# Optimization experiments

Measured on AMD Instinct MI355X. Metric: run time of the kernel, lower is better.

The kernel has to match this reference:

```python
import jax, jax.numpy as jnp
import numpy as np

N, F_IN, H, C, D, NH, L, FF = 4096, 256, 2, 64, 128, 4, 2, 2048
DEG = 32


def setup_inputs() -> dict:
    key = jax.random.key(0)
    ks = jax.random.split(key, 32)
    s = 0.05
    # graph: random edges + self loops (PyG GATConv adds self loops)
    src = jax.random.randint(ks[0], (N * DEG,), 0, N)
    dst = jax.random.randint(ks[1], (N * DEG,), 0, N)
    loop = jnp.arange(N)
    edge_index = jnp.stack([jnp.concatenate([src, loop]),
                            jnp.concatenate([dst, loop])]).astype(jnp.int64)
    inp = {
        'x': jax.random.normal(ks[2], (N, F_IN), jnp.float32),
        'edge_index': edge_index,
        'enc_w1': jax.random.normal(ks[3], (F_IN, 128), jnp.float32) * s,
        'enc_b1': jnp.zeros((128,), jnp.float32),
        'enc_w2': jax.random.normal(ks[4], (128, D), jnp.float32) * s,
        'enc_b2': jnp.zeros((D,), jnp.float32),
        'gat_w': jax.random.normal(ks[5], (D, H * C), jnp.float32) * s,
        'gat_asrc': jax.random.normal(ks[6], (H, C), jnp.float32) * s,
        'gat_adst': jax.random.normal(ks[7], (H, C), jnp.float32) * s,
        'gat_bias': jnp.zeros((H * C,), jnp.float32),
        't_wq': jax.random.normal(ks[8], (L, D, D), jnp.float32) * s,
        't_bq': jnp.zeros((L, D), jnp.float32),
        't_wk': jax.random.normal(ks[9], (L, D, D), jnp.float32) * s,
        't_bk': jnp.zeros((L, D), jnp.float32),
        't_wv': jax.random.normal(ks[10], (L, D, D), jnp.float32) * s,
        't_bv': jnp.zeros((L, D), jnp.float32),
        't_wo': jax.random.normal(ks[11], (L, D, D), jnp.float32) * s,
        't_bo': jnp.zeros((L, D), jnp.float32),
        't_ln1_g': jnp.ones((L, D), jnp.float32),
        't_ln1_b': jnp.zeros((L, D), jnp.float32),
        't_ln2_g': jnp.ones((L, D), jnp.float32),
        't_ln2_b': jnp.zeros((L, D), jnp.float32),
        't_w1': jax.random.normal(ks[12], (L, D, FF), jnp.float32) * s,
        't_b1': jnp.zeros((L, FF), jnp.float32),
        't_w2': jax.random.normal(ks[13], (L, FF, D), jnp.float32) * s,
        't_b2': jnp.zeros((L, D), jnp.float32),
    }
    return inp


def _layer_norm(v, g, b):
    m = v.mean(-1, keepdims=True)
    var = v.var(-1, keepdims=True)
    return (v - m) / jnp.sqrt(var + 1e-5) * g + b


def _forward(x, edge_index, enc_w1, enc_b1, enc_w2, enc_b2,
             gat_w, gat_asrc, gat_adst, gat_bias,
             t_wq, t_bq, t_wk, t_bk, t_wv, t_bv, t_wo, t_bo,
             t_ln1_g, t_ln1_b, t_ln2_g, t_ln2_b, t_w1, t_b1, t_w2, t_b2):
    n = x.shape[0]
    # encoder MLP: Linear -> ReLU -> Linear
    h = jnp.maximum(x @ enc_w1 + enc_b1, 0.0) @ enc_w2 + enc_b2  # [N, D]
    # GATConv (concat heads), dropout inactive (eval)
    heads, ch = gat_asrc.shape
    hh = (h @ gat_w).reshape(n, heads, ch)                       # [N, H, C]
    src, dst = edge_index[0], edge_index[1]
    a_src = (hh * gat_asrc).sum(-1)                              # [N, H]
    a_dst = (hh * gat_adst).sum(-1)
    e = jax.nn.leaky_relu(a_src[src] + a_dst[dst], 0.2)          # [E, H]
    # segment softmax over destination nodes
    e_max = jax.ops.segment_max(e, dst, num_segments=n)
    e_exp = jnp.exp(e - e_max[dst])
    denom = jax.ops.segment_sum(e_exp, dst, num_segments=n)
    alpha = e_exp / denom[dst]                                   # [E, H]
    agg = jax.ops.segment_sum(alpha[:, :, None] * hh[src], dst, num_segments=n)
    y = agg.reshape(n, heads * ch) + gat_bias                    # [N, D]
    # TransformerEncoder (post-LN, relu FFN), unbatched sequence of N nodes
    d = y.shape[-1]
    dh = d // NH
    for l in range(t_wq.shape[0]):
        q = (y @ t_wq[l] + t_bq[l]).reshape(n, NH, dh)
        k = (y @ t_wk[l] + t_bk[l]).reshape(n, NH, dh)
        v = (y @ t_wv[l] + t_bv[l]).reshape(n, NH, dh)
        scores = jnp.einsum('nhd,mhd->hnm', q, k) / jnp.sqrt(jnp.float32(dh))
        p = jax.nn.softmax(scores, axis=-1)
        a = jnp.einsum('hnm,mhd->nhd', p, v).reshape(n, d)
        a = a @ t_wo[l] + t_bo[l]
        y = _layer_norm(y + a, t_ln1_g[l], t_ln1_b[l])
        f = jnp.maximum(y @ t_w1[l] + t_b1[l], 0.0) @ t_w2[l] + t_b2[l]
        y = _layer_norm(y + f, t_ln2_g[l], t_ln2_b[l])
    return y


def reference(x, edge_index, enc_w1, enc_b1, enc_w2, enc_b2,
              gat_w, gat_asrc, gat_adst, gat_bias,
              t_wq, t_bq, t_wk, t_bk, t_wv, t_bv, t_wo, t_bo,
              t_ln1_g, t_ln1_b, t_ln2_g, t_ln2_b, t_w1, t_b1, t_w2, t_b2):
    return _forward(x, edge_index, enc_w1, enc_b1, enc_w2, enc_b2,
                    gat_w, gat_asrc, gat_adst, gat_bias,
                    t_wq, t_bq, t_wk, t_bk, t_wv, t_bv, t_wo, t_bo,
                    t_ln1_g, t_ln1_b, t_ln2_g, t_ln2_b, t_w1, t_b1, t_w2, t_b2)
```

## Files before the change

kernel.cpp:

```cpp
#include <hip/hip_runtime.h>

typedef unsigned short u16;
typedef unsigned int u32;
typedef __attribute__((ext_vector_type(8))) short bh8;
typedef __attribute__((ext_vector_type(4))) float fx4;
typedef __attribute__((ext_vector_type(4))) short s4;
typedef __attribute__((ext_vector_type(2))) unsigned int u32x2;

#define QS 0.2550437194342803f

__device__ __forceinline__ u16 f2bf(float f) {
    unsigned u = __float_as_uint(f);
    u += 0x7fffu + ((u >> 16) & 1u);
    return (u16)(u >> 16);
}

__device__ __forceinline__ u32 cvtpk(float lo, float hi) {
    u32 r;
    asm("v_cvt_pk_bf16_f32 %0, %1, %2" : "=v"(r) : "v"(lo), "v"(hi));
    return r;
}

__global__ __launch_bounds__(256) void prep_kernel(
    const float* x, const float* ew1, const float* ew2, const float* gw,
    const float* wq, const float* wk, const float* wv, const float* wo,
    const float* w1, const float* w2,
    const float* bq, const float* bk, const float* bv,
    u16* xb, u16* ew1t, u16* ew2t, u16* gwt,
    u16* wqkvt, float* bqkv, u16* wot, u16* w1t, u16* w2t)
{
    __shared__ u16 tile[64 * 65];
    int bid = blockIdx.x;
    const int t = threadIdx.x;

    if (bid < 128) {
        const float4* x4 = (const float4*)x;
        s4* o4 = (s4*)xb;
        #pragma unroll
        for (int i = 0; i < 8; i++) {
            int fi = bid * 2048 + i * 256 + t;
            float4 v = x4[fi];
            s4 o = { (short)f2bf(v.x), (short)f2bf(v.y), (short)f2bf(v.z), (short)f2bf(v.w) };
            o4[fi] = o;
        }
        return;
    }
    bid -= 128;
    if (bid < 1) {
        for (int idx = t; idx < 768; idx += 256) {
            int l = idx / 384, n = idx % 384;
            float v;
            if (n < 128)      v = bq[l * 128 + n] * QS;
            else if (n < 256) v = bk[l * 128 + n - 128];
            else              v = bv[l * 128 + n - 256];
            bqkv[idx] = v;
        }
        return;
    }
    bid -= 1;

    const float* src; u16* dst; int R, C, tr, tc; float sc = 1.f;
    if (bid < 8)            { src = ew1; dst = ew1t; R = 256; C = 128; tr = bid >> 1; tc = bid & 1; }
    else if ((bid -= 8) < 4)  { src = ew2; dst = ew2t; R = 128; C = 128; tr = bid >> 1; tc = bid & 1; }
    else if ((bid -= 4) < 4)  { src = gw;  dst = gwt;  R = 128; C = 128; tr = bid >> 1; tc = bid & 1; }
    else if ((bid -= 4) < 24) {
        int l = bid / 12, r2 = bid % 12, which = r2 >> 2, i = r2 & 3;
        R = 128; C = 128; tr = i >> 1; tc = i & 1;
        if (which == 0)      { src = wq + l * 16384; dst = wqkvt + l * 49152;         sc = QS; }
        else if (which == 1) { src = wk + l * 16384; dst = wqkvt + l * 49152 + 16384; }
        else                 { src = wv + l * 16384; dst = wqkvt + l * 49152 + 32768; }
    }
    else if ((bid -= 24) < 8)   { int l = bid >> 2, i = bid & 3;  src = wo + l * 16384; dst = wot + l * 16384; R = 128; C = 128; tr = i >> 1; tc = i & 1; }
    else if ((bid -= 8) < 128)  { int l = bid >> 6, i = bid & 63; src = w1 + (size_t)l * 262144; dst = w1t + (size_t)l * 262144; R = 128;  C = 2048; tr = i & 1;  tc = i >> 1; }
    else { bid -= 128;            int l = bid >> 6, i = bid & 63; src = w2 + (size_t)l * 262144; dst = w2t + (size_t)l * 262144; R = 2048; C = 128;  tr = i >> 1; tc = i & 1; }

    const int r = t >> 2, cs = (t & 3) * 16;
    const float* sp = src + (size_t)(tr * 64 + r) * C + tc * 64 + cs;
    #pragma unroll
    for (int j = 0; j < 16; j++) tile[r * 65 + cs + j] = f2bf(sp[j] * sc);
    __syncthreads();
    u16* dp = dst + (size_t)(tc * 64 + r) * R + tr * 64 + cs;
    #pragma unroll
    for (int j = 0; j < 16; j++) dp[j] = tile[(cs + j) * 65 + r];
}

__global__ __launch_bounds__(256) void gemm_bf16(
    const u16* __restrict__ A, const u16* __restrict__ Bt,
    const float* __restrict__ bias,
    float* __restrict__ Cf, u16* __restrict__ Cb, float* __restrict__ Cpart,
    u16* __restrict__ Cvt,
    int M, int N, int K, int relu, int kchunk, int ldc)
{
    __shared__ __align__(16) u16 As[2][64][40];
    __shared__ __align__(16) u16 Bs[2][64][40];
    const int m0 = blockIdx.x * 64, n0 = blockIdx.y * 64, z = blockIdx.z;
    const int tid = threadIdx.x;
    const int lane = tid & 63, w = tid >> 6;
    const int wm = (w >> 1) * 32, wn = (w & 1) * 32;
    const int l15 = lane & 15, l4 = lane >> 4;
    const int srow = tid >> 2, skq = (tid & 3) * 8;
    const int k0 = z * kchunk;

    const u16* Ap = A + (size_t)(m0 + srow) * K + k0 + skq;
    const u16* Bp = Bt + (size_t)(n0 + srow) * K + k0 + skq;

    fx4 acc00 = {0,0,0,0}, acc01 = {0,0,0,0}, acc10 = {0,0,0,0}, acc11 = {0,0,0,0};

    *(int4*)&As[0][srow][skq] = *(const int4*)Ap;
    *(int4*)&Bs[0][srow][skq] = *(const int4*)Bp;

    const int niter = kchunk >> 5;
    for (int it = 0; it < niter; it++) {
        const int cur = it & 1;
        int4 ar, br;
        __syncthreads();
        if (it + 1 < niter) {
            ar = *(const int4*)(Ap + (it + 1) * 32);
            br = *(const int4*)(Bp + (it + 1) * 32);
        }
        bh8 a0 = *(const bh8*)&As[cur][wm + l15][l4 * 8];
        bh8 a1 = *(const bh8*)&As[cur][wm + 16 + l15][l4 * 8];
        bh8 b0 = *(const bh8*)&Bs[cur][wn + l15][l4 * 8];
        bh8 b1 = *(const bh8*)&Bs[cur][wn + 16 + l15][l4 * 8];
        acc00 = __builtin_amdgcn_mfma_f32_16x16x32_bf16(a0, b0, acc00, 0, 0, 0);
        acc01 = __builtin_amdgcn_mfma_f32_16x16x32_bf16(a0, b1, acc01, 0, 0, 0);
        acc10 = __builtin_amdgcn_mfma_f32_16x16x32_bf16(a1, b0, acc10, 0, 0, 0);
        acc11 = __builtin_amdgcn_mfma_f32_16x16x32_bf16(a1, b1, acc11, 0, 0, 0);
        if (it + 1 < niter) {
            *(int4*)&As[cur ^ 1][srow][skq] = ar;
            *(int4*)&Bs[cur ^ 1][srow][skq] = br;
        }
    }

    fx4* accs[2][2] = {{&acc00, &acc01}, {&acc10, &acc11}};
    #pragma unroll
    for (int i = 0; i < 2; i++)
        #pragma unroll
        for (int j = 0; j < 2; j++) {
            int colg = n0 + wn + j * 16 + l15;
            int rowb = m0 + wm + i * 16 + l4 * 4;
            if (Cpart) {
                float* cp = Cpart + (size_t)z * M * N;
                #pragma unroll
                for (int r = 0; r < 4; r++)
                    cp[(size_t)(rowb + r) * N + colg] = (*accs[i][j])[r];
                continue;
            }
            float bvv = bias ? bias[colg] : 0.f;
            float vals[4];
            #pragma unroll
            for (int r = 0; r < 4; r++) {
                float v = (*accs[i][j])[r] + bvv;
                vals[r] = relu ? fmaxf(v, 0.f) : v;
            }
            if (Cvt && colg >= 256) {
                s4 pk = { (short)f2bf(vals[0]), (short)f2bf(vals[1]),
                          (short)f2bf(vals[2]), (short)f2bf(vals[3]) };
                *(s4*)&Cvt[(size_t)(colg - 256) * 4096 + rowb] = pk;
            } else {
                #pragma unroll
                for (int r = 0; r < 4; r++) {
                    if (Cf) Cf[(size_t)(rowb + r) * ldc + colg] = vals[r];
                    if (Cb) Cb[(size_t)(rowb + r) * ldc + colg] = f2bf(vals[r]);
                }
            }
        }
}

__global__ __launch_bounds__(128) void gat_prep(
    const float* __restrict__ hh, const float* __restrict__ asrc,
    const float* __restrict__ adst, float* __restrict__ an_src,
    float* __restrict__ an_dst, int* __restrict__ counts)
{
    int n = blockIdx.x, tid = threadIdx.x;
    if (tid == 0) counts[n] = 0;
    int head = tid >> 6, c = tid & 63;
    float v = hh[n * 128 + tid];
    float ps = v * asrc[head * 64 + c];
    float pd = v * adst[head * 64 + c];
    for (int off = 32; off; off >>= 1) { ps += __shfl_down(ps, off); pd += __shfl_down(pd, off); }
    if (c == 0) { an_src[n * 2 + head] = ps; an_dst[n * 2 + head] = pd; }
}

__global__ void count_edges(const int* __restrict__ dst, int* counts, int E) {
    int i = blockIdx.x * 256 + threadIdx.x;
    if (i < E) atomicAdd(&counts[dst[i]], 1);
}

__global__ __launch_bounds__(1024) void scan_kernel(const int* __restrict__ counts,
                                                    int* row_start, int* cursor) {
    __shared__ int wsum[16];
    int tid = threadIdx.x, lane = tid & 63, wv = tid >> 6;
    int b = tid * 4;
    int c0 = counts[b], c1 = counts[b+1], c2 = counts[b+2], c3 = counts[b+3];
    int sum = c0 + c1 + c2 + c3;
    int inc = sum;
    #pragma unroll
    for (int off = 1; off < 64; off <<= 1) {
        int v = __shfl_up(inc, off);
        if (lane >= off) inc += v;
    }
    if (lane == 63) wsum[wv] = inc;
    __syncthreads();
    int base = 0;
    #pragma unroll
    for (int i = 0; i < 16; i++) {
        int v = wsum[i];
        base += (i < wv) ? v : 0;
    }
    int excl = base + inc - sum;
    int r0 = excl, r1 = excl + c0, r2 = r1 + c1, r3 = r2 + c2;
    row_start[b] = r0; row_start[b+1] = r1; row_start[b+2] = r2; row_start[b+3] = r3;
    cursor[b] = r0; cursor[b+1] = r1; cursor[b+2] = r2; cursor[b+3] = r3;
    if (tid == 1023) row_start[4096] = base + inc;
}

__global__ void scatter_edges(const int* __restrict__ src, const int* __restrict__ dst,
                              int* cursor, int* csr_src, int E) {
    int i = blockIdx.x * 256 + threadIdx.x;
    if (i < E) { int pos = atomicAdd(&cursor[dst[i]], 1); csr_src[pos] = src[i]; }
}

__global__ __launch_bounds__(256) void gat_aggregate(
    const int* __restrict__ row_start, const int* __restrict__ csr_src,
    const float* __restrict__ an_src, const float* __restrict__ an_dst,
    const float* __restrict__ hh, const float* __restrict__ gbias,
    float* __restrict__ y32, u16* __restrict__ yb)
{
    int n = blockIdx.x, tid = threadIdx.x;
    const int lane = tid & 63, wv = tid >> 6;
    int start = row_start[n], end = row_start[n + 1];
    float ad0 = an_dst[n * 2 + 0], ad1 = an_dst[n * 2 + 1];
    __shared__ float rmx[4][2], rsm[4][2];
    __shared__ float sal0[128], sal1[128], sagg[256];
    __shared__ int sidx[128];

    float mx0 = -1e30f, mx1 = -1e30f;
    for (int i = start + tid; i < end; i += 256) {
        int s = csr_src[i];
        float e0 = an_src[s * 2 + 0] + ad0; e0 = e0 > 0.f ? e0 : 0.2f * e0;
        float e1 = an_src[s * 2 + 1] + ad1; e1 = e1 > 0.f ? e1 : 0.2f * e1;
        mx0 = fmaxf(mx0, e0); mx1 = fmaxf(mx1, e1);
    }
    for (int off = 32; off; off >>= 1) { mx0 = fmaxf(mx0, __shfl_down(mx0, off)); mx1 = fmaxf(mx1, __shfl_down(mx1, off)); }
    if (lane == 0) { rmx[wv][0] = mx0; rmx[wv][1] = mx1; }
    __syncthreads();
    mx0 = fmaxf(fmaxf(rmx[0][0], rmx[1][0]), fmaxf(rmx[2][0], rmx[3][0]));
    mx1 = fmaxf(fmaxf(rmx[0][1], rmx[1][1]), fmaxf(rmx[2][1], rmx[3][1]));

    float den0 = 0.f, den1 = 0.f;
    for (int i = start + tid; i < end; i += 256) {
        int s = csr_src[i];
        float e0 = an_src[s * 2 + 0] + ad0; e0 = e0 > 0.f ? e0 : 0.2f * e0;
        float e1 = an_src[s * 2 + 1] + ad1; e1 = e1 > 0.f ? e1 : 0.2f * e1;
        den0 += __expf(e0 - mx0); den1 += __expf(e1 - mx1);
    }
    for (int off = 32; off; off >>= 1) { den0 += __shfl_down(den0, off); den1 += __shfl_down(den1, off); }
    if (lane == 0) { rsm[wv][0] = den0; rsm[wv][1] = den1; }
    __syncthreads();
    den0 = rsm[0][0] + rsm[1][0] + rsm[2][0] + rsm[3][0];
    den1 = rsm[0][1] + rsm[1][1] + rsm[2][1] + rsm[3][1];
    float rd0 = 1.f / den0, rd1 = 1.f / den1;

    const int grp = tid >> 7, ch = tid & 127, head = ch >> 6;
    float agg = 0.f;
    for (int c0 = start; c0 < end; c0 += 128) {
        int cnt = min(128, end - c0);
        __syncthreads();
        if (tid < cnt) {
            int s = csr_src[c0 + tid];
            float e0 = an_src[s * 2 + 0] + ad0; e0 = e0 > 0.f ? e0 : 0.2f * e0;
            float e1 = an_src[s * 2 + 1] + ad1; e1 = e1 > 0.f ? e1 : 0.2f * e1;
            sal0[tid] = __expf(e0 - mx0) * rd0;
            sal1[tid] = __expf(e1 - mx1) * rd1;
            sidx[tid] = s;
        }
        __syncthreads();
        const float* sal = head ? sal1 : sal0;
        for (int j = grp; j < cnt; j += 2)
            agg += sal[j] * hh[(size_t)sidx[j] * 128 + ch];
    }
    sagg[tid] = agg;
    __syncthreads();
    if (tid < 128) {
        float v = sagg[tid] + sagg[tid + 128] + gbias[tid];
        y32[(size_t)n * 128 + tid] = v;
        yb[(size_t)n * 128 + tid] = f2bf(v);
    }
}

__global__ __launch_bounds__(256) void flash_attn_part(
    const u16* __restrict__ q, const u16* __restrict__ k,
    const u16* __restrict__ vt, float* __restrict__ po,
    float* __restrict__ pm, float* __restrict__ pl)
{
    __shared__ __align__(16) u16 Kb[2][64][40];
    __shared__ __align__(16) u16 Vb[2][32][72];
    __shared__ __align__(16) u16 Ps[4][16][72];
    const int q0 = blockIdx.x * 64, h = blockIdx.y, ch = blockIdx.z;
    const int tid = threadIdx.x;
    const int w = tid >> 6, lane = tid & 63, l15 = lane & 15, l4 = lane >> 4;

    bh8 qf = *(const bh8*)&q[(size_t)(q0 + w * 16 + l15) * 256 + h * 32 + l4 * 8];

    const int skey = tid >> 2, sds = (tid & 3) * 8;
    const int svd = tid >> 3, svk = (tid & 7) * 8;
    const u16* kgp = &k[(size_t)(ch * 512 + skey) * 256 + h * 32 + sds];
    const u16* vgp = &vt[(size_t)(h * 32 + svd) * 4096 + ch * 512 + svk];

    fx4 o0 = {0,0,0,0}, o1 = {0,0,0,0};
    float M = -1e30f, L = 0.f;

    *(int4*)&Kb[0][skey][sds] = *(const int4*)kgp;
    *(int4*)&Vb[0][svd][svk] = *(const int4*)vgp;

    for (int ti = 0; ti < 8; ti++) {
        const int cur = ti & 1;
        int4 kr, vr;
        __syncthreads();
        if (ti < 7) {
            kr = *(const int4*)(kgp + (size_t)(ti + 1) * 64 * 256);
            vr = *(const int4*)(vgp + (ti + 1) * 64);
        }

        fx4 s[4];
        #pragma unroll
        for (int sub = 0; sub < 4; sub++) {
            bh8 kf = *(const bh8*)&Kb[cur][sub * 16 + l15][l4 * 8];
            fx4 z = {0,0,0,0};
            s[sub] = __builtin_amdgcn_mfma_f32_16x16x32_bf16(kf, qf, z, 0, 0, 0);
        }
        float t0 = fmaxf(fmaxf(s[0][0], s[0][1]), s[0][2]);
        float t1 = fmaxf(fmaxf(s[0][3], s[1][0]), s[1][1]);
        float t2 = fmaxf(fmaxf(s[1][2], s[1][3]), s[2][0]);
        float t3 = fmaxf(fmaxf(s[2][1], s[2][2]), s[2][3]);
        float t4 = fmaxf(fmaxf(s[3][0], s[3][1]), s[3][2]);
        float pmax = fmaxf(fmaxf(fmaxf(t0, t1), t2), fmaxf(fmaxf(t3, t4), s[3][3]));
        pmax = fmaxf(pmax, __shfl_xor(pmax, 16));
        pmax = fmaxf(pmax, __shfl_xor(pmax, 32));
        if (!__all(pmax - M <= 8.0f)) {
            float f = __builtin_amdgcn_exp2f(M - pmax);
            M = pmax;
            o0 *= f; o1 *= f; L *= f;
        }

        #pragma unroll
        for (int sub = 0; sub < 4; sub++)
            #pragma unroll
            for (int r = 0; r < 4; r++)
                s[sub][r] = __builtin_amdgcn_exp2f(s[sub][r] - M);
        float ss0 = (s[0][0] + s[0][1]) + (s[0][2] + s[0][3]);
        float ss1 = (s[1][0] + s[1][1]) + (s[1][2] + s[1][3]);
        float ss2 = (s[2][0] + s[2][1]) + (s[2][2] + s[2][3]);
        float ss3 = (s[3][0] + s[3][1]) + (s[3][2] + s[3][3]);
        float lsum = (ss0 + ss1) + (ss2 + ss3);
        lsum += __shfl_xor(lsum, 16);
        lsum += __shfl_xor(lsum, 32);
        L += lsum;

        #pragma unroll
        for (int sub = 0; sub < 4; sub++) {
            u32x2 pk = { cvtpk(s[sub][0], s[sub][1]), cvtpk(s[sub][2], s[sub][3]) };
            *(u32x2*)&Ps[w][l15][sub * 16 + l4 * 4] = pk;
        }

        #pragma unroll
        for (int kc = 0; kc < 2; kc++) {
            bh8 bf  = *(const bh8*)&Ps[w][l15][kc * 32 + l4 * 8];
            bh8 af0 = *(const bh8*)&Vb[cur][l15][kc * 32 + l4 * 8];
            bh8 af1 = *(const bh8*)&Vb[cur][16 + l15][kc * 32 + l4 * 8];
            o0 = __builtin_amdgcn_mfma_f32_16x16x32_bf16(af0, bf, o0, 0, 0, 0);
            o1 = __builtin_amdgcn_mfma_f32_16x16x32_bf16(af1, bf, o1, 0, 0, 0);
        }

        if (ti < 7) {
            *(int4*)&Kb[cur ^ 1][skey][sds] = kr;
            *(int4*)&Vb[cur ^ 1][svd][svk] = vr;
        }
    }
    const int base = (blockIdx.x * 4 + h) * 8 + ch;
    const int qrow = w * 16 + l15;
    *(fx4*)&po[(size_t)(base * 64 + qrow) * 32 + l4 * 4]      = o0;
    *(fx4*)&po[(size_t)(base * 64 + qrow) * 32 + 16 + l4 * 4] = o1;
    if (l4 == 0) { pm[base * 64 + qrow] = M; pl[base * 64 + qrow] = L; }
}

__global__ __launch_bounds__(256) void attn_combine(
    const float* __restrict__ po, const float* __restrict__ pm,
    const float* __restrict__ pl, u16* __restrict__ out)
{
    int qb = blockIdx.x, h = blockIdx.y;
    int col = threadIdx.x & 31, r0 = threadIdx.x >> 5;
    int rb = (qb * 4 + h) * 8;
    for (int j = 0; j < 8; j++) {
        int row = r0 * 8 + j;
        float m = -1e30f;
        for (int c = 0; c < 8; c++) m = fmaxf(m, pm[(rb + c) * 64 + row]);
        float l = 0.f, o = 0.f;
        for (int c = 0; c < 8; c++) {
            float wgt = __builtin_amdgcn_exp2f(pm[(rb + c) * 64 + row] - m);
            l += wgt * pl[(rb + c) * 64 + row];
            o += wgt * po[(size_t)((rb + c) * 64 + row) * 32 + col];
        }
        out[(size_t)(qb * 64 + row) * 128 + h * 32 + col] = f2bf(o / l);
    }
}

__global__ __launch_bounds__(256) void oproj_ln(
    const u16* __restrict__ A, const u16* __restrict__ Bt,
    const float* __restrict__ bias, const float* __restrict__ g,
    const float* __restrict__ b,
    float* __restrict__ y32, u16* __restrict__ yb)
{
    __shared__ __align__(16) u16 As[2][32][40];
    __shared__ __align__(16) u16 Bs[2][128][40];
    __shared__ float Ct[32][132];
    const int m0 = blockIdx.x * 32;
    const int tid = threadIdx.x;
    const int lane = tid & 63, w = tid >> 6;
    const int wm = (w >> 1) * 16, wn = (w & 1) * 64;
    const int l15 = lane & 15, l4 = lane >> 4;

    const int arow = tid >> 2, akq = (tid & 3) * 8;
    const u16* Ap  = A + (size_t)(m0 + arow) * 128 + akq;
    const u16* Bp0 = Bt + (size_t)arow * 128 + akq;
    const u16* Bp1 = Bp0 + (size_t)64 * 128;

    fx4 acc[4] = {};

    if (tid < 128) *(int4*)&As[0][arow][akq] = *(const int4*)Ap;
    *(int4*)&Bs[0][arow][akq]      = *(const int4*)Bp0;
    *(int4*)&Bs[0][arow + 64][akq] = *(const int4*)Bp1;

    for (int it = 0; it < 4; it++) {
        const int cur = it & 1;
        int4 ar, br0, br1;
        __syncthreads();
        if (it < 3) {
            if (tid < 128) ar = *(const int4*)(Ap + (it + 1) * 32);
            br0 = *(const int4*)(Bp0 + (it + 1) * 32);
            br1 = *(const int4*)(Bp1 + (it + 1) * 32);
        }
        bh8 af = *(const bh8*)&As[cur][wm + l15][l4 * 8];
        #pragma unroll
        for (int nj = 0; nj < 4; nj++) {
            bh8 bf = *(const bh8*)&Bs[cur][wn + nj * 16 + l15][l4 * 8];
            acc[nj] = __builtin_amdgcn_mfma_f32_16x16x32_bf16(af, bf, acc[nj], 0, 0, 0);
        }
        if (it < 3) {
            if (tid < 128) *(int4*)&As[cur ^ 1][arow][akq] = ar;
            *(int4*)&Bs[cur ^ 1][arow][akq]      = br0;
            *(int4*)&Bs[cur ^ 1][arow + 64][akq] = br1;
        }
    }

    #pragma unroll
    for (int nj = 0; nj < 4; nj++) {
        int cl = wn + nj * 16 + l15;
        float bvv = bias[cl];
        #pragma unroll
        for (int r = 0; r < 4; r++) {
            int rl = wm + l4 * 4 + r;
            Ct[rl][cl] = acc[nj][r] + bvv + y32[(size_t)(m0 + rl) * 128 + cl];
        }
    }
    __syncthreads();

    const int row = tid >> 3, c0 = (tid & 7) * 16;
    float s1 = 0.f, s2 = 0.f;
    #pragma unroll
    for (int j = 0; j < 16; j++) { float v = Ct[row][c0 + j]; s1 += v; s2 += v * v; }
    #pragma unroll
    for (int off = 1; off < 8; off <<= 1) { s1 += __shfl_xor(s1, off); s2 += __shfl_xor(s2, off); }
    float mean = s1 * (1.f / 128.f);
    float var = s2 * (1.f / 128.f) - mean * mean;
    float rstd = rsqrtf(var + 1e-5f);
    #pragma unroll
    for (int j = 0; j < 16; j++) {
        int col = c0 + j;
        float o = (Ct[row][col] - mean) * rstd * g[col] + b[col];
        y32[(size_t)(m0 + row) * 128 + col] = o;
        yb[(size_t)(m0 + row) * 128 + col] = f2bf(o);
    }
}

__global__ __launch_bounds__(128) void add_ln_p(
    const float* __restrict__ y, const float* __restrict__ part, int nz,
    const float* __restrict__ bias,
    const float* __restrict__ g, const float* __restrict__ b,
    float* __restrict__ out32, u16* __restrict__ outb)
{
    int n = blockIdx.x, tid = threadIdx.x;
    float v = y[(size_t)n * 128 + tid] + bias[tid];
    for (int z = 0; z < nz; z++) v += part[(size_t)z * 524288 + n * 128 + tid];
    float sacc = v;
    for (int off = 32; off; off >>= 1) sacc += __shfl_down(sacc, off);
    __shared__ float sm[2], sv[2];
    if ((tid & 63) == 0) sm[tid >> 6] = sacc;
    __syncthreads();
    float mean = (sm[0] + sm[1]) * (1.f / 128.f);
    float d = v - mean;
    float qacc = d * d;
    for (int off = 32; off; off >>= 1) qacc += __shfl_down(qacc, off);
    if ((tid & 63) == 0) sv[tid >> 6] = qacc;
    __syncthreads();
    float var = (sv[0] + sv[1]) * (1.f / 128.f);
    float o = d * rsqrtf(var + 1e-5f) * g[tid] + b[tid];
    out32[(size_t)n * 128 + tid] = o;
    outb[(size_t)n * 128 + tid] = f2bf(o);
}

extern "C" void kernel_launch(void* const* d_in, const int* in_sizes, int n_in,
                              void* d_out, int out_size, void* d_ws, size_t ws_size,
                              hipStream_t stream)
{
    const float* x     = (const float*)d_in[0];
    const int*   ei    = (const int*)  d_in[1];
    const float* ew1   = (const float*)d_in[2];
    const float* eb1   = (const float*)d_in[3];
    const float* ew2   = (const float*)d_in[4];
    const float* eb2   = (const float*)d_in[5];
    const float* gw    = (const float*)d_in[6];
    const float* gasrc = (const float*)d_in[7];
    const float* gadst = (const float*)d_in[8];
    const float* gbias = (const float*)d_in[9];
    const float* wq    = (const float*)d_in[10];
    const float* bq    = (const float*)d_in[11];
    const float* wk    = (const float*)d_in[12];
    const float* bk    = (const float*)d_in[13];
    const float* wv    = (const float*)d_in[14];
    const float* bv    = (const float*)d_in[15];
    const float* wo    = (const float*)d_in[16];
    const float* bo    = (const float*)d_in[17];
    const float* ln1g  = (const float*)d_in[18];
    const float* ln1b  = (const float*)d_in[19];
    const float* ln2g  = (const float*)d_in[20];
    const float* ln2b  = (const float*)d_in[21];
    const float* w1    = (const float*)d_in[22];
    const float* b1    = (const float*)d_in[23];
    const float* w2    = (const float*)d_in[24];
    const float* b2    = (const float*)d_in[25];

    const int E = in_sizes[1] / 2;
    const int* esrc = ei;
    const int* edst = ei + E;

    char* p = (char*)d_ws;
    auto alloc = [&](size_t bytes) -> void* {
        void* r = (void*)p;
        p += (bytes + 255) & ~(size_t)255;
        return r;
    };
    u16* xb    = (u16*)alloc(4096 * 256 * 2);
    u16* ew1t  = (u16*)alloc(128 * 256 * 2);
    u16* ew2t  = (u16*)alloc(128 * 128 * 2);
    u16* gwt   = (u16*)alloc(128 * 128 * 2);
    u16* wqkvt = (u16*)alloc(2 * 384 * 128 * 2);
    float* bqkv = (float*)alloc(2 * 384 * 4);
    u16* wot   = (u16*)alloc(2 * 128 * 128 * 2);
    u16* w1t   = (u16*)alloc(2 * 2048 * 128 * 2);
    u16* w2t   = (u16*)alloc(2 * 128 * 2048 * 2);
    u16* h1b   = (u16*)alloc(4096 * 128 * 2);
    u16* hb    = (u16*)alloc(4096 * 128 * 2);
    float* hh  = (float*)alloc(4096 * 128 * 4);
    float* ansrc = (float*)alloc(4096 * 2 * 4);
    float* andst = (float*)alloc(4096 * 2 * 4);
    int* counts    = (int*)alloc(4096 * 4);
    int* row_start = (int*)alloc(4097 * 4);
    int* cursor    = (int*)alloc(4096 * 4);
    int* csr_src   = (int*)alloc((size_t)E * 4);
    float* y32 = (float*)alloc(4096 * 128 * 4);
    u16* yb    = (u16*)alloc(4096 * 128 * 2);
    u16* qkvb  = (u16*)alloc((size_t)4096 * 256 * 2);
    u16* vtb   = (u16*)alloc(4096 * 128 * 2);
    u16* attnb = (u16*)alloc(4096 * 128 * 2);
    float* po  = (float*)alloc((size_t)64 * 4 * 8 * 64 * 32 * 4);
    float* pm  = (float*)alloc(64 * 4 * 8 * 64 * 4);
    float* pl  = (float*)alloc(64 * 4 * 8 * 64 * 4);
    u16* ff1b  = (u16*)alloc((size_t)4096 * 2048 * 2);
    float* ff2part = (float*)alloc((size_t)4 * 4096 * 128 * 4);

    prep_kernel<<<433, 256, 0, stream>>>(x, ew1, ew2, gw, wq, wk, wv, wo, w1, w2,
                                         bq, bk, bv,
                                         xb, ew1t, ew2t, gwt, wqkvt, bqkv, wot, w1t, w2t);

    gemm_bf16<<<dim3(64, 2), 256, 0, stream>>>(xb, ew1t, eb1, nullptr, h1b, nullptr, nullptr, 4096, 128, 256, 1, 256, 128);
    gemm_bf16<<<dim3(64, 2), 256, 0, stream>>>(h1b, ew2t, eb2, nullptr, hb, nullptr, nullptr, 4096, 128, 128, 0, 128, 128);

    gemm_bf16<<<dim3(64, 2), 256, 0, stream>>>(hb, gwt, nullptr, hh, nullptr, nullptr, nullptr, 4096, 128, 128, 0, 128, 128);
    gat_prep<<<4096, 128, 0, stream>>>(hh, gasrc, gadst, ansrc, andst, counts);
    count_edges<<<(E + 255) / 256, 256, 0, stream>>>(edst, counts, E);
    scan_kernel<<<1, 1024, 0, stream>>>(counts, row_start, cursor);
    scatter_edges<<<(E + 255) / 256, 256, 0, stream>>>(esrc, edst, cursor, csr_src, E);
    gat_aggregate<<<4096, 256, 0, stream>>>(row_start, csr_src, ansrc, andst, hh, gbias, y32, yb);

    for (int l = 0; l < 2; l++) {
        gemm_bf16<<<dim3(64, 6), 256, 0, stream>>>(yb, wqkvt + l * 49152, bqkv + l * 384, nullptr, qkvb, nullptr, vtb, 4096, 384, 128, 0, 128, 256);
        flash_attn_part<<<dim3(64, 4, 8), 256, 0, stream>>>(qkvb, qkvb + 128, vtb, po, pm, pl);
        attn_combine<<<dim3(64, 4), 256, 0, stream>>>(po, pm, pl, attnb);
        oproj_ln<<<128, 256, 0, stream>>>(attnb, wot + l * 16384, bo + l * 128, ln1g + l * 128, ln1b + l * 128, y32, yb);
        gemm_bf16<<<dim3(64, 32), 256, 0, stream>>>(yb, w1t + (size_t)l * 262144, b1 + l * 2048, nullptr, ff1b, nullptr, nullptr, 4096, 2048, 128, 1, 128, 2048);
        gemm_bf16<<<dim3(64, 2, 4), 256, 0, stream>>>(ff1b, w2t + (size_t)l * 262144, nullptr, nullptr, nullptr, ff2part, nullptr, 4096, 128, 2048, 0, 512, 128);
        float* outp = (l == 1) ? (float*)d_out : y32;
        add_ln_p<<<4096, 128, 0, stream>>>(y32, ff2part, 4, b2 + l * 128, ln2g + l * 128, ln2b + l * 128, outp, yb);
    }
}
```

Before: 199.6 us.

## Fuse FFN up/down projections into one kernel and halve attention key splits

Adds an ffn_fused kernel in which each block keeps a 64-row activation tile in LDS. It computes ReLU(yW1+b1) for 64-wide FF chunks into shared memory and multiplies them directly by W2, writing 8 split-K partial sums. This removes the 4096x2048 bf16 intermediate round-trip to global memory and one launch, but W2 fragments are read straight from global and the partial-sum traffic doubles. Separately, flash attention now uses 4 key chunks of 1024 instead of 8 of 512, which cuts combine work and partial buffers but halves grid parallelism.

```diff
diff --git a/kernel.cpp b/kernel.cpp
--- a/kernel.cpp
+++ b/kernel.cpp
@@ -167,6 +167,94 @@
         }
 }
 
+__global__ __launch_bounds__(256) void ffn_fused(
+    const u16* __restrict__ A, const u16* __restrict__ W1t,
+    const float* __restrict__ b1, const u16* __restrict__ W2t,
+    float* __restrict__ part)
+{
+    __shared__ __align__(16) u16 Ab[64][136];
+    __shared__ __align__(16) u16 Wb[64][136];
+    __shared__ __align__(16) u16 Sb[64][72];
+    const int m0 = blockIdx.x * 64, z = blockIdx.y;
+    const int tid = threadIdx.x;
+    const int lane = tid & 63, w = tid >> 6;
+    const int wm = (w >> 1) * 32;
+    const int wn = (w & 1) * 32;
+    const int wn2 = (w & 1) * 64;
+    const int l15 = lane & 15, l4 = lane >> 4;
+    const int sr = tid >> 2, sc = (tid & 3) * 32;
+
+    {
+        const u16* ap = A + (size_t)(m0 + sr) * 128 + sc;
+        #pragma unroll
+        for (int i = 0; i < 4; i++)
+            *(int4*)&Ab[sr][sc + i * 8] = *(const int4*)(ap + i * 8);
+    }
+
+    fx4 acc2[2][4] = {};
+
+    for (int chunk = 0; chunk < 4; chunk++) {
+        const int ffbase = z * 256 + chunk * 64;
+        __syncthreads();
+        {
+            const u16* wp = W1t + (size_t)(ffbase + sr) * 128 + sc;
+            #pragma unroll
+            for (int i = 0; i < 4; i++)
+                *(int4*)&Wb[sr][sc + i * 8] = *(const int4*)(wp + i * 8);
+        }
+        __syncthreads();
+
+        fx4 s[2][2] = {};
+        #pragma unroll
+        for (int ks = 0; ks < 4; ks++) {
+            bh8 af0 = *(const bh8*)&Ab[wm + l15][ks * 32 + l4 * 8];
+            bh8 af1 = *(const bh8*)&Ab[wm + 16 + l15][ks * 32 + l4 * 8];
+            bh8 bf0 = *(const bh8*)&Wb[wn + l15][ks * 32 + l4 * 8];
+            bh8 bf1 = *(const bh8*)&Wb[wn + 16 + l15][ks * 32 + l4 * 8];
+            s[0][0] = __builtin_amdgcn_mfma_f32_16x16x32_bf16(af0, bf0, s[0][0], 0, 0, 0);
+            s[0][1] = __builtin_amdgcn_mfma_f32_16x16x32_bf16(af0, bf1, s[0][1], 0, 0, 0);
+            s[1][0] = __builtin_amdgcn_mfma_f32_16x16x32_bf16(af1, bf0, s[1][0], 0, 0, 0);
+            s[1][1] = __builtin_amdgcn_mfma_f32_16x16x32_bf16(af1, bf1, s[1][1], 0, 0, 0);
+        }
+        #pragma unroll
+        for (int mi = 0; mi < 2; mi++)
+            #pragma unroll
+            for (int nj = 0; nj < 2; nj++) {
+                float bv = b1[ffbase + wn + nj * 16 + l15];
+                #pragma unroll
+                for (int r = 0; r < 4; r++) {
+                    float v = fmaxf(s[mi][nj][r] + bv, 0.f);
+                    Sb[wm + mi * 16 + l4 * 4 + r][wn + nj * 16 + l15] = f2bf(v);
+                }
+            }
+        __syncthreads();
+
+        #pragma unroll
+        for (int ks = 0; ks < 2; ks++) {
+            bh8 af0 = *(const bh8*)&Sb[wm + l15][ks * 32 + l4 * 8];
+            bh8 af1 = *(const bh8*)&Sb[wm + 16 + l15][ks * 32 + l4 * 8];
+            #pragma unroll
+            for (int nj = 0; nj < 4; nj++) {
+                bh8 bf = *(const bh8*)&W2t[(size_t)(wn2 + nj * 16 + l15) * 2048 + ffbase + ks * 32 + l4 * 8];
+                acc2[0][nj] = __builtin_amdgcn_mfma_f32_16x16x32_bf16(af0, bf, acc2[0][nj], 0, 0, 0);
+                acc2[1][nj] = __builtin_amdgcn_mfma_f32_16x16x32_bf16(af1, bf, acc2[1][nj], 0, 0, 0);
+            }
+        }
+    }
+
+    float* cp = part + (size_t)z * 524288;
+    #pragma unroll
+    for (int mi = 0; mi < 2; mi++)
+        #pragma unroll
+        for (int nj = 0; nj < 4; nj++) {
+            int colg = wn2 + nj * 16 + l15;
+            int rowb = m0 + wm + mi * 16 + l4 * 4;
+            #pragma unroll
+            for (int r = 0; r < 4; r++)
+                cp[(size_t)(rowb + r) * 128 + colg] = acc2[mi][nj][r];
+        }
+}
+
 __global__ __launch_bounds__(128) void gat_prep(
     const float* __restrict__ hh, const float* __restrict__ asrc,
     const float* __restrict__ adst, float* __restrict__ an_src,
@@ -305,8 +393,8 @@
 
     const int skey = tid >> 2, sds = (tid & 3) * 8;
     const int svd = tid >> 3, svk = (tid & 7) * 8;
-    const u16* kgp = &k[(size_t)(ch * 512 + skey) * 256 + h * 32 + sds];
-    const u16* vgp = &vt[(size_t)(h * 32 + svd) * 4096 + ch * 512 + svk];
+    const u16* kgp = &k[(size_t)(ch * 1024 + skey) * 256 + h * 32 + sds];
+    const u16* vgp = &vt[(size_t)(h * 32 + svd) * 4096 + ch * 1024 + svk];
 
     fx4 o0 = {0,0,0,0}, o1 = {0,0,0,0};
     float M = -1e30f, L = 0.f;
@@ -314,11 +402,11 @@
     *(int4*)&Kb[0][skey][sds] = *(const int4*)kgp;
     *(int4*)&Vb[0][svd][svk] = *(const int4*)vgp;
 
-    for (int ti = 0; ti < 8; ti++) {
+    for (int ti = 0; ti < 16; ti++) {
         const int cur = ti & 1;
         int4 kr, vr;
         __syncthreads();
-        if (ti < 7) {
+        if (ti < 15) {
             kr = *(const int4*)(kgp + (size_t)(ti + 1) * 64 * 256);
             vr = *(const int4*)(vgp + (ti + 1) * 64);
         }
@@ -373,12 +461,12 @@
             o1 = __builtin_amdgcn_mfma_f32_16x16x32_bf16(af1, bf, o1, 0, 0, 0);
         }
 
-        if (ti < 7) {
+        if (ti < 15) {
             *(int4*)&Kb[cur ^ 1][skey][sds] = kr;
             *(int4*)&Vb[cur ^ 1][svd][svk] = vr;
         }
     }
-    const int base = (blockIdx.x * 4 + h) * 8 + ch;
+    const int base = (blockIdx.x * 4 + h) * 4 + ch;
     const int qrow = w * 16 + l15;
     *(fx4*)&po[(size_t)(base * 64 + qrow) * 32 + l4 * 4]      = o0;
     *(fx4*)&po[(size_t)(base * 64 + qrow) * 32 + 16 + l4 * 4] = o1;
@@ -391,13 +479,13 @@
 {
     int qb = blockIdx.x, h = blockIdx.y;
     int col = threadIdx.x & 31, r0 = threadIdx.x >> 5;
-    int rb = (qb * 4 + h) * 8;
+    int rb = (qb * 4 + h) * 4;
     for (int j = 0; j < 8; j++) {
         int row = r0 * 8 + j;
         float m = -1e30f;
-        for (int c = 0; c < 8; c++) m = fmaxf(m, pm[(rb + c) * 64 + row]);
+        for (int c = 0; c < 4; c++) m = fmaxf(m, pm[(rb + c) * 64 + row]);
         float l = 0.f, o = 0.f;
-        for (int c = 0; c < 8; c++) {
+        for (int c = 0; c < 4; c++) {
             float wgt = __builtin_amdgcn_exp2f(pm[(rb + c) * 64 + row] - m);
             l += wgt * pl[(rb + c) * 64 + row];
             o += wgt * po[(size_t)((rb + c) * 64 + row) * 32 + col];
@@ -574,11 +662,10 @@
     u16* qkvb  = (u16*)alloc((size_t)4096 * 256 * 2);
     u16* vtb   = (u16*)alloc(4096 * 128 * 2);
     u16* attnb = (u16*)alloc(4096 * 128 * 2);
-    float* po  = (float*)alloc((size_t)64 * 4 * 8 * 64 * 32 * 4);
-    float* pm  = (float*)alloc(64 * 4 * 8 * 64 * 4);
-    float* pl  = (float*)alloc(64 * 4 * 8 * 64 * 4);
-    u16* ff1b  = (u16*)alloc((size_t)4096 * 2048 * 2);
-    float* ff2part = (float*)alloc((size_t)4 * 4096 * 128 * 4);
+    float* po  = (float*)alloc((size_t)64 * 4 * 4 * 64 * 32 * 4);
+    float* pm  = (float*)alloc(64 * 4 * 4 * 64 * 4);
+    float* pl  = (float*)alloc(64 * 4 * 4 * 64 * 4);
+    float* ffpart = (float*)alloc((size_t)8 * 4096 * 128 * 4);
 
     prep_kernel<<<433, 256, 0, stream>>>(x, ew1, ew2, gw, wq, wk, wv, wo, w1, w2,
                                          bq, bk, bv,
@@ -596,12 +683,11 @@
 
     for (int l = 0; l < 2; l++) {
         gemm_bf16<<<dim3(64, 6), 256, 0, stream>>>(yb, wqkvt + l * 49152, bqkv + l * 384, nullptr, qkvb, nullptr, vtb, 4096, 384, 128, 0, 128, 256);
-        flash_attn_part<<<dim3(64, 4, 8), 256, 0, stream>>>(qkvb, qkvb + 128, vtb, po, pm, pl);
+        flash_attn_part<<<dim3(64, 4, 4), 256, 0, stream>>>(qkvb, qkvb + 128, vtb, po, pm, pl);
         attn_combine<<<dim3(64, 4), 256, 0, stream>>>(po, pm, pl, attnb);
         oproj_ln<<<128, 256, 0, stream>>>(attnb, wot + l * 16384, bo + l * 128, ln1g + l * 128, ln1b + l * 128, y32, yb);
-        gemm_bf16<<<dim3(64, 32), 256, 0, stream>>>(yb, w1t + (size_t)l * 262144, b1 + l * 2048, nullptr, ff1b, nullptr, nullptr, 4096, 2048, 128, 1, 128, 2048);
-        gemm_bf16<<<dim3(64, 2, 4), 256, 0, stream>>>(ff1b, w2t + (size_t)l * 262144, nullptr, nullptr, nullptr, ff2part, nullptr, 4096, 128, 2048, 0, 512, 128);
+        ffn_fused<<<dim3(64, 8), 256, 0, stream>>>(yb, w1t + (size_t)l * 262144, b1 + l * 2048, w2t + (size_t)l * 262144, ffpart);
         float* outp = (l == 1) ? (float*)d_out : y32;
-        add_ln_p<<<4096, 128, 0, stream>>>(y32, ff2part, 4, b2 + l * 128, ln2g + l * 128, ln2b + l * 128, outp, yb);
-    }
-}
+        add_ln_p<<<4096, 128, 0, stream>>>(y32, ffpart, 8, b2 + l * 128, ln2g + l * 128, ln2b + l * 128, outp, yb);
+    }
+}
```

Result: faster. 195.4 us (-2.1%).
